# Kernel optimization log

Measured on AMD Instinct MI355X. Metric: run time of the kernel, lower is better.

Reference implementation:

```python
import jax, jax.numpy as jnp
import numpy as np

RADIUS = 1.0 / 16.0
MAX_NEIGHBORS = 64  # forward() passes max_num_neighbors=64
N_POINTS = 16384
N_CLOUDS = 8


def _radius_neighbors(pos, batch, r, k):
    """Dense radius graph: for each point, up to k in-radius same-cloud neighbors.
    Returns idx [N,k] int32 and mask [N,k] bool. loop=True -> self always valid."""
    sq = jnp.sum(pos * pos, axis=-1)                        # [N]
    d2 = sq[:, None] + sq[None, :] - 2.0 * (pos @ pos.T)    # [N,N]
    d2 = jnp.maximum(d2, 0.0)
    valid = (d2 <= r * r) & (batch[:, None] == batch[None, :])
    score = jnp.where(valid, -d2, -jnp.inf)
    vals, idx = jax.lax.top_k(score, k)                     # nearest-first, [N,k]
    mask = vals > -jnp.inf
    return idx, mask


def _point_conv(x, pos, idx, mask, W1, b1, W2, b2):
    """PointNetConv: msg = relu(Linear([x_j, pos_j - pos_i])), max-agg, Linear."""
    xj = x[idx]                                   # [N,K,c_in]  gather
    rel = pos[idx] - pos[:, None, :]              # [N,K,3]
    h = jnp.concatenate([xj, rel], axis=-1) @ W1 + b1   # [N,K,c_mid]
    h = jax.nn.relu(h)
    h = jnp.where(mask[..., None], h, -jnp.inf)
    agg = jnp.max(h, axis=1)                      # [N,c_mid]  max aggregation
    agg = jnp.where(jnp.isfinite(agg), agg, 0.0)  # safety (loop=True makes this moot)
    return agg @ W2 + b2                          # [N,c_out]


def setup_inputs() -> dict:
    key = jax.random.key(0)
    ks = jax.random.split(key, 16)
    pos = jax.random.uniform(ks[0], (N_POINTS, 3), dtype=jnp.float32)
    rgb = jax.random.uniform(ks[1], (N_POINTS, 3), dtype=jnp.float32)
    batch = jnp.sort(jax.random.randint(ks[2], (N_POINTS,), 0, N_CLOUDS)).astype(jnp.int64)

    def lin(k, fan_in, fan_out):
        kw, kb = jax.random.split(k)
        bound = 1.0 / np.sqrt(fan_in)
        W = jax.random.uniform(kw, (fan_in, fan_out), jnp.float32, -bound, bound)
        b = jax.random.uniform(kb, (fan_out,), jnp.float32, -bound, bound)
        return W, b

    W1a, b1a = lin(ks[3], 3 + 3, 8)
    W2a, b2a = lin(ks[4], 8, 8)
    W1b, b1b = lin(ks[5], 8 + 3, 16)
    W2b, b2b = lin(ks[6], 16, 16)
    W1c, b1c = lin(ks[7], 16 + 3, 32)
    W2c, b2c = lin(ks[8], 32, 32)
    return {"pos": pos, "rgb": rgb, "batch": batch,
            "W1a": W1a, "b1a": b1a, "W2a": W2a, "b2a": b2a,
            "W1b": W1b, "b1b": b1b, "W2b": W2b, "b2b": b2b,
            "W1c": W1c, "b1c": b1c, "W2c": W2c, "b2c": b2c}


def reference(pos, rgb, batch,
              W1a, b1a, W2a, b2a,
              W1b, b1b, W2b, b2b,
              W1c, b1c, W2c, b2c):
    # NOTE: rgb is accepted by the original forward() but never used.
    idx, mask = _radius_neighbors(pos, batch, RADIUS, MAX_NEIGHBORS)
    out = jax.nn.celu(_point_conv(pos, pos, idx, mask, W1a, b1a, W2a, b2a))
    out = jax.nn.celu(_point_conv(out, pos, idx, mask, W1b, b1b, W2b, b2b))
    out = jax.nn.celu(_point_conv(out, pos, idx, mask, W1c, b1c, W2c, b2c))
    return pos, out, batch
```

## Files before the change

### kernel.cpp

```cpp
#include <hip/hip_runtime.h>
#include <math.h>

#define N_POINTS 16384
#define CELLS_PER_CLOUD 4096
#define N_CELLS 32768
#define CAP 16
#define NBR_STRIDE 32

constexpr double R2D = 1.0 / 256.0;

__global__ __launch_bounds__(256) void k_prep(const float* __restrict__ pos,
                                              const int* __restrict__ batch,
                                              float* __restrict__ out,
                                              int* __restrict__ cnt,
                                              float4* __restrict__ bucket,
                                              float4* __restrict__ pos4)
{
    int i = blockIdx.x * 256 + threadIdx.x;
    out[i]                = pos[i];
    out[i + N_POINTS]     = pos[i + N_POINTS];
    out[i + 2 * N_POINTS] = pos[i + 2 * N_POINTS];
    out[3 * N_POINTS + 32 * N_POINTS + i] = (float)batch[i];

    float x = pos[3 * i], y = pos[3 * i + 1], z = pos[3 * i + 2];
    int ix = min(max((int)(x * 16.f), 0), 15);
    int iy = min(max((int)(y * 16.f), 0), 15);
    int iz = min(max((int)(z * 16.f), 0), 15);
    int cell = ((batch[i] * 16 + iz) * 16 + iy) * 16 + ix;
    pos4[i] = make_float4(x, y, z, __int_as_float(cell));
    int slot = atomicAdd(&cnt[cell], 1);
    if (slot < CAP) bucket[cell * CAP + slot] = make_float4(x, y, z, __int_as_float(i));
}

__global__ __launch_bounds__(512) void k_search_a(
    const float4* __restrict__ pos4,
    const int* __restrict__ cnt, const float4* __restrict__ bucket,
    const float* __restrict__ W1, const float* __restrict__ b1,
    const float* __restrict__ W2, const float* __restrict__ b2,
    float* __restrict__ out_a, float4* __restrict__ nbr, int* __restrict__ nbr_cnt)
{
    __shared__ float sW1[48], sB1[8], sW2[64], sB2[8];
    __shared__ float4 s_hits[NBR_STRIDE][64];
    __shared__ int s_k[64];

    int t = threadIdx.x;
    int p = t & 63;
    int g = t >> 6;

    if (t < 48) sW1[t] = W1[t];
    if (t < 8) { sB1[t] = b1[t]; sB2[t] = b2[t]; }
    if (t < 64) { sW2[t] = W2[t]; s_k[t] = 0; }
    __syncthreads();

    int i = blockIdx.x * 64 + p;
    float4 pi4 = pos4[i];
    float xi = pi4.x, yi = pi4.y, zi = pi4.z;
    double xd = (double)xi, yd = (double)yi, zd = (double)zi;
    int cell0 = __float_as_int(pi4.w);
    int ix = cell0 & 15, iy = (cell0 >> 4) & 15, iz = (cell0 >> 8) & 15;
    int cb = cell0 & ~(CELLS_PER_CLOUD - 1);

    int n[4], cid[4];
#pragma unroll
    for (int cc = 0; cc < 4; cc++) {
        int c = g + 8 * cc;
        int dz = c / 9 - 1, dy = (c / 3) % 3 - 1, dx = c % 3 - 1;
        int zz = iz + dz, yy = iy + dy, xx = ix + dx;
        bool ok = (c < 27) & ((zz | yy | xx) >= 0) & (zz < 16) & (yy < 16) & (xx < 16);
        int zc = min(max(zz, 0), 15), yc = min(max(yy, 0), 15),
            xc = min(max(xx, 0), 15);
        cid[cc] = cb + (zc << 8) + (yc << 4) + xc;
        int nc = min(cnt[cid[cc]], CAP);
        n[cc] = ok ? nc : 0;
    }
    int nmax = 0;
#pragma unroll
    for (int cc = 0; cc < 4; cc++) nmax = max(nmax, n[cc]);

    for (int s = 0; s < nmax; s++) {
#pragma unroll
        for (int cc = 0; cc < 4; cc++) {
            if (s < n[cc]) {
                float4 q = bucket[cid[cc] * CAP + s];
                double ddx = xd - (double)q.x, ddy = yd - (double)q.y,
                       ddz = zd - (double)q.z;
                double d2 = ddx * ddx + ddy * ddy + ddz * ddz;
                if (d2 <= R2D) {
                    int slot = atomicAdd(&s_k[p], 1);
                    if (slot < NBR_STRIDE) {
                        s_hits[slot][p] = q;
                        nbr[i * NBR_STRIDE + slot] = q;
                    }
                }
            }
        }
    }
    __syncthreads();

    if (g == 0) {
        int kc = min(s_k[p], NBR_STRIDE);
        nbr_cnt[i] = kc;

        float mx[8];
#pragma unroll
        for (int m = 0; m < 8; m++) mx[m] = 0.f;
        for (int kk = 0; kk < kc; kk++) {
            float4 q = s_hits[kk][p];
            float in6[6] = { q.x, q.y, q.z, q.x - xi, q.y - yi, q.z - zi };
#pragma unroll
            for (int m = 0; m < 8; m++) {
                float h = sB1[m];
#pragma unroll
                for (int c6 = 0; c6 < 6; c6++) h = fmaf(in6[c6], sW1[c6 * 8 + m], h);
                mx[m] = fmaxf(mx[m], fmaxf(h, 0.f));
            }
        }

        float o[8];
#pragma unroll
        for (int m = 0; m < 8; m++) {
            float v = sB2[m];
#pragma unroll
            for (int kk = 0; kk < 8; kk++) v = fmaf(mx[kk], sW2[kk * 8 + m], v);
            o[m] = v > 0.f ? v : expm1f(v);
        }
        *(float4*)&out_a[i * 8]     = make_float4(o[0], o[1], o[2], o[3]);
        *(float4*)&out_a[i * 8 + 4] = make_float4(o[4], o[5], o[6], o[7]);
    }
}

template<int CIN4, int CMID, int PTS>
__global__ __launch_bounds__(256) void k_conv(
    const float4* __restrict__ pos4, const float4* __restrict__ xin4,
    const float4* __restrict__ nbr, const int* __restrict__ nbr_cnt,
    const float* __restrict__ W1, const float* __restrict__ b1,
    const float* __restrict__ W2, const float* __restrict__ b2,
    float* __restrict__ xout)
{
    constexpr int CIN = CIN4 * 4;
    __shared__ float4 s_q[PTS][NBR_STRIDE];
    __shared__ float4 s_x[PTS][NBR_STRIDE][CIN4];
    __shared__ float  s_agg[PTS][CMID + 1];

    int tid = threadIdx.x;

#pragma unroll
    for (int w = tid; w < PTS * NBR_STRIDE; w += 256) {
        int sp = w >> 5, slot = w & 31;
        int si = blockIdx.x * PTS + sp;
        if (slot < nbr_cnt[si]) {
            float4 q = nbr[si * NBR_STRIDE + slot];
            s_q[sp][slot] = q;
            int j = __float_as_int(q.w);
#pragma unroll
            for (int k = 0; k < CIN4; k++) s_x[sp][slot][k] = xin4[j * CIN4 + k];
        }
    }
    __syncthreads();

    int p = tid / CMID;
    int m = tid % CMID;
    int i = blockIdx.x * PTS + p;

    float4 pi = pos4[i];
    int cnt = nbr_cnt[i];

    float w1c[CIN + 3];
#pragma unroll
    for (int k = 0; k < CIN + 3; k++) w1c[k] = W1[k * CMID + m];
    float w2c[CMID];
#pragma unroll
    for (int k = 0; k < CMID; k++) w2c[k] = W2[k * CMID + m];
    float bb = b1[m];

    float mxv = 0.f;
    for (int t = 0; t < cnt; t++) {
        float4 q = s_q[p][t];
        float h = bb;
#pragma unroll
        for (int k = 0; k < CIN4; k++) {
            float4 v = s_x[p][t][k];
            h = fmaf(v.x, w1c[4 * k],     h);
            h = fmaf(v.y, w1c[4 * k + 1], h);
            h = fmaf(v.z, w1c[4 * k + 2], h);
            h = fmaf(v.w, w1c[4 * k + 3], h);
        }
        h = fmaf(q.x - pi.x, w1c[CIN],     h);
        h = fmaf(q.y - pi.y, w1c[CIN + 1], h);
        h = fmaf(q.z - pi.z, w1c[CIN + 2], h);
        mxv = fmaxf(mxv, fmaxf(h, 0.f));
    }
    s_agg[p][m] = mxv;
    __syncthreads();

    float o = b2[m];
#pragma unroll
    for (int k = 0; k < CMID; k++) o = fmaf(s_agg[p][k], w2c[k], o);
    xout[i * CMID + m] = o > 0.f ? o : expm1f(o);
}

extern "C" void kernel_launch(void* const* d_in, const int* in_sizes, int n_in,
                              void* d_out, int out_size, void* d_ws, size_t ws_size,
                              hipStream_t stream)
{
    const float* pos   = (const float*)d_in[0];
    const int*   batch = (const int*)d_in[2];
    const float* W1a = (const float*)d_in[3];
    const float* b1a = (const float*)d_in[4];
    const float* W2a = (const float*)d_in[5];
    const float* b2a = (const float*)d_in[6];
    const float* W1b = (const float*)d_in[7];
    const float* b1b = (const float*)d_in[8];
    const float* W2b = (const float*)d_in[9];
    const float* b2b = (const float*)d_in[10];
    const float* W1c = (const float*)d_in[11];
    const float* b1c = (const float*)d_in[12];
    const float* W2c = (const float*)d_in[13];
    const float* b2c = (const float*)d_in[14];

    float* out = (float*)d_out;

    char* ws = (char*)d_ws;
    size_t off = 0;
    auto alloc = [&](size_t bytes) {
        char* p = ws + off; off += (bytes + 255) & ~size_t(255); return p;
    };
    int*    cnt     = (int*)alloc(N_CELLS * 4);
    float4* bucket  = (float4*)alloc((size_t)N_CELLS * CAP * 16);
    float4* pos4    = (float4*)alloc(N_POINTS * 16);
    int*    nbr_cnt = (int*)alloc(N_POINTS * 4);
    float4* nbr     = (float4*)alloc((size_t)N_POINTS * NBR_STRIDE * 16);
    float*  out_a   = (float*)alloc(N_POINTS * 8 * 4);
    float*  out_b   = (float*)alloc(N_POINTS * 16 * 4);

    hipMemsetAsync(cnt, 0, N_CELLS * 4, stream);
    hipLaunchKernelGGL(k_prep, dim3(N_POINTS / 256), dim3(256), 0, stream,
                       pos, batch, out, cnt, bucket, pos4);
    hipLaunchKernelGGL(k_search_a, dim3(N_POINTS / 64), dim3(512), 0, stream,
                       pos4, cnt, bucket, W1a, b1a, W2a, b2a,
                       out_a, nbr, nbr_cnt);
    hipLaunchKernelGGL((k_conv<2, 16, 16>), dim3(N_POINTS / 16), dim3(256), 0, stream,
                       pos4, (const float4*)out_a, nbr, nbr_cnt,
                       W1b, b1b, W2b, b2b, out_b);
    hipLaunchKernelGGL((k_conv<4, 32, 8>), dim3(N_POINTS / 8), dim3(256), 0, stream,
                       pos4, (const float4*)out_b, nbr, nbr_cnt,
                       W1c, b1c, W2c, b2c, out + 3 * N_POINTS);
}
```

Baseline: 112.5 us.

## Split neighbor search across more threads and replace memset with in-kernel reset

Halves the points per search block so each thread scans two neighbor cells instead of four, and spreads the first-layer MLP across eight threads per point using shared memory for the max-aggregated values. The cell-count buffer becomes a device global that the final conv kernel zeroes, which removes the separate memset launch. This relies on the zero-initialised global and stream ordering across calls, and adds an extra barrier in the search kernel.

```diff
diff --git a/kernel.cpp b/kernel.cpp
--- a/kernel.cpp
+++ b/kernel.cpp
@@ -9,10 +9,11 @@
 
 constexpr double R2D = 1.0 / 256.0;
 
+__device__ int g_cnt[N_CELLS];
+
 __global__ __launch_bounds__(256) void k_prep(const float* __restrict__ pos,
                                               const int* __restrict__ batch,
                                               float* __restrict__ out,
-                                              int* __restrict__ cnt,
                                               float4* __restrict__ bucket,
                                               float4* __restrict__ pos4)
 {
@@ -28,31 +29,32 @@
     int iz = min(max((int)(z * 16.f), 0), 15);
     int cell = ((batch[i] * 16 + iz) * 16 + iy) * 16 + ix;
     pos4[i] = make_float4(x, y, z, __int_as_float(cell));
-    int slot = atomicAdd(&cnt[cell], 1);
+    int slot = atomicAdd(&g_cnt[cell], 1);
     if (slot < CAP) bucket[cell * CAP + slot] = make_float4(x, y, z, __int_as_float(i));
 }
 
 __global__ __launch_bounds__(512) void k_search_a(
-    const float4* __restrict__ pos4,
-    const int* __restrict__ cnt, const float4* __restrict__ bucket,
+    const float4* __restrict__ pos4, const float4* __restrict__ bucket,
     const float* __restrict__ W1, const float* __restrict__ b1,
     const float* __restrict__ W2, const float* __restrict__ b2,
     float* __restrict__ out_a, float4* __restrict__ nbr, int* __restrict__ nbr_cnt)
 {
     __shared__ float sW1[48], sB1[8], sW2[64], sB2[8];
-    __shared__ float4 s_hits[NBR_STRIDE][64];
-    __shared__ int s_k[64];
+    __shared__ float4 s_hits[NBR_STRIDE][32];
+    __shared__ int   s_k[32];
+    __shared__ float s_mx[32][9];
 
     int t = threadIdx.x;
-    int p = t & 63;
-    int g = t >> 6;
+    int p = t & 31;
+    int g = t >> 5;
 
     if (t < 48) sW1[t] = W1[t];
     if (t < 8) { sB1[t] = b1[t]; sB2[t] = b2[t]; }
-    if (t < 64) { sW2[t] = W2[t]; s_k[t] = 0; }
-    __syncthreads();
-
-    int i = blockIdx.x * 64 + p;
+    if (t < 64) sW2[t] = W2[t];
+    if (t < 32) s_k[t] = 0;
+    __syncthreads();
+
+    int i = blockIdx.x * 32 + p;
     float4 pi4 = pos4[i];
     float xi = pi4.x, yi = pi4.y, zi = pi4.z;
     double xd = (double)xi, yd = (double)yi, zd = (double)zi;
@@ -60,26 +62,24 @@
     int ix = cell0 & 15, iy = (cell0 >> 4) & 15, iz = (cell0 >> 8) & 15;
     int cb = cell0 & ~(CELLS_PER_CLOUD - 1);
 
-    int n[4], cid[4];
-#pragma unroll
-    for (int cc = 0; cc < 4; cc++) {
-        int c = g + 8 * cc;
+    int n[2], cid[2];
+#pragma unroll
+    for (int cc = 0; cc < 2; cc++) {
+        int c = g + 16 * cc;
         int dz = c / 9 - 1, dy = (c / 3) % 3 - 1, dx = c % 3 - 1;
         int zz = iz + dz, yy = iy + dy, xx = ix + dx;
         bool ok = (c < 27) & ((zz | yy | xx) >= 0) & (zz < 16) & (yy < 16) & (xx < 16);
         int zc = min(max(zz, 0), 15), yc = min(max(yy, 0), 15),
             xc = min(max(xx, 0), 15);
         cid[cc] = cb + (zc << 8) + (yc << 4) + xc;
-        int nc = min(cnt[cid[cc]], CAP);
+        int nc = min(g_cnt[cid[cc]], CAP);
         n[cc] = ok ? nc : 0;
     }
-    int nmax = 0;
-#pragma unroll
-    for (int cc = 0; cc < 4; cc++) nmax = max(nmax, n[cc]);
+    int nmax = max(n[0], n[1]);
 
     for (int s = 0; s < nmax; s++) {
 #pragma unroll
-        for (int cc = 0; cc < 4; cc++) {
+        for (int cc = 0; cc < 2; cc++) {
             if (s < n[cc]) {
                 float4 q = bucket[cid[cc] * CAP + s];
                 double ddx = xd - (double)q.x, ddy = yd - (double)q.y,
@@ -96,40 +96,32 @@
         }
     }
     __syncthreads();
-
-    if (g == 0) {
-        int kc = min(s_k[p], NBR_STRIDE);
-        nbr_cnt[i] = kc;
-
-        float mx[8];
-#pragma unroll
-        for (int m = 0; m < 8; m++) mx[m] = 0.f;
+    int kc = min(s_k[p], NBR_STRIDE);
+
+    if (g == 0) nbr_cnt[i] = kc;
+
+    if (g < 8) {
+        float mxv = 0.f;
         for (int kk = 0; kk < kc; kk++) {
             float4 q = s_hits[kk][p];
             float in6[6] = { q.x, q.y, q.z, q.x - xi, q.y - yi, q.z - zi };
-#pragma unroll
-            for (int m = 0; m < 8; m++) {
-                float h = sB1[m];
-#pragma unroll
-                for (int c6 = 0; c6 < 6; c6++) h = fmaf(in6[c6], sW1[c6 * 8 + m], h);
-                mx[m] = fmaxf(mx[m], fmaxf(h, 0.f));
-            }
-        }
-
-        float o[8];
-#pragma unroll
-        for (int m = 0; m < 8; m++) {
-            float v = sB2[m];
-#pragma unroll
-            for (int kk = 0; kk < 8; kk++) v = fmaf(mx[kk], sW2[kk * 8 + m], v);
-            o[m] = v > 0.f ? v : expm1f(v);
-        }
-        *(float4*)&out_a[i * 8]     = make_float4(o[0], o[1], o[2], o[3]);
-        *(float4*)&out_a[i * 8 + 4] = make_float4(o[4], o[5], o[6], o[7]);
-    }
-}
-
-template<int CIN4, int CMID, int PTS>
+            float h = sB1[g];
+#pragma unroll
+            for (int c6 = 0; c6 < 6; c6++) h = fmaf(in6[c6], sW1[c6 * 8 + g], h);
+            mxv = fmaxf(mxv, fmaxf(h, 0.f));
+        }
+        s_mx[p][g] = mxv;
+    }
+    __syncthreads();
+    if (g < 8) {
+        float o = sB2[g];
+#pragma unroll
+        for (int k = 0; k < 8; k++) o = fmaf(s_mx[p][k], sW2[k * 8 + g], o);
+        out_a[i * 8 + g] = o > 0.f ? o : expm1f(o);
+    }
+}
+
+template<int CIN4, int CMID, int PTS, bool ZERO_CNT>
 __global__ __launch_bounds__(256) void k_conv(
     const float4* __restrict__ pos4, const float4* __restrict__ xin4,
     const float4* __restrict__ nbr, const int* __restrict__ nbr_cnt,
@@ -143,6 +135,11 @@
     __shared__ float  s_agg[PTS][CMID + 1];
 
     int tid = threadIdx.x;
+
+    if (ZERO_CNT) {
+        int gid = blockIdx.x * 256 + tid;
+        if (gid < N_CELLS) g_cnt[gid] = 0;
+    }
 
 #pragma unroll
     for (int w = tid; w < PTS * NBR_STRIDE; w += 256) {
@@ -225,7 +222,6 @@
     auto alloc = [&](size_t bytes) {
         char* p = ws + off; off += (bytes + 255) & ~size_t(255); return p;
     };
-    int*    cnt     = (int*)alloc(N_CELLS * 4);
     float4* bucket  = (float4*)alloc((size_t)N_CELLS * CAP * 16);
     float4* pos4    = (float4*)alloc(N_POINTS * 16);
     int*    nbr_cnt = (int*)alloc(N_POINTS * 4);
@@ -233,16 +229,15 @@
     float*  out_a   = (float*)alloc(N_POINTS * 8 * 4);
     float*  out_b   = (float*)alloc(N_POINTS * 16 * 4);
 
-    hipMemsetAsync(cnt, 0, N_CELLS * 4, stream);
     hipLaunchKernelGGL(k_prep, dim3(N_POINTS / 256), dim3(256), 0, stream,
-                       pos, batch, out, cnt, bucket, pos4);
-    hipLaunchKernelGGL(k_search_a, dim3(N_POINTS / 64), dim3(512), 0, stream,
-                       pos4, cnt, bucket, W1a, b1a, W2a, b2a,
+                       pos, batch, out, bucket, pos4);
+    hipLaunchKernelGGL(k_search_a, dim3(N_POINTS / 32), dim3(512), 0, stream,
+                       pos4, bucket, W1a, b1a, W2a, b2a,
                        out_a, nbr, nbr_cnt);
-    hipLaunchKernelGGL((k_conv<2, 16, 16>), dim3(N_POINTS / 16), dim3(256), 0, stream,
+    hipLaunchKernelGGL((k_conv<2, 16, 16, false>), dim3(N_POINTS / 16), dim3(256), 0, stream,
                        pos4, (const float4*)out_a, nbr, nbr_cnt,
                        W1b, b1b, W2b, b2b, out_b);
-    hipLaunchKernelGGL((k_conv<4, 32, 8>), dim3(N_POINTS / 8), dim3(256), 0, stream,
+    hipLaunchKernelGGL((k_conv<4, 32, 8, true>), dim3(N_POINTS / 8), dim3(256), 0, stream,
                        pos4, (const float4*)out_b, nbr, nbr_cnt,
                        W1c, b1c, W2c, b2c, out + 3 * N_POINTS);
 }
```

After: 110.4 us (median of 2 runs). About the same (-1.9%).
